# Optimization experiments

Hardware: AMD Instinct MI355X
Metric: run time of the kernel (lower is better)

The kernel has to match this reference:

```python
import jax, jax.numpy as jnp
import numpy as np

B, N, T, F = 8, 2000, 64, 32
H = 128    # lstm_hidden
GH = 128   # gnn_hidden
E = 32000  # edges


def setup_inputs() -> dict:
    key = jax.random.key(0)
    ks = jax.random.split(key, 12)
    s = 0.05
    return {
        "x": jax.random.normal(ks[0], (B, N, T, F), jnp.float32),
        "edge_index": jax.random.randint(ks[1], (2, E), 0, N, dtype=jnp.int32),
        # LSTM params (torch gate order i, f, g, o)
        "Wih": jax.random.normal(ks[2], (4 * H, F), jnp.float32) * s,
        "Whh": jax.random.normal(ks[3], (4 * H, H), jnp.float32) * s,
        "bih": jax.random.normal(ks[4], (4 * H,), jnp.float32) * s,
        "bhh": jax.random.normal(ks[5], (4 * H,), jnp.float32) * s,
        # GCNConv params
        "gcn_W": jax.random.normal(ks[6], (H, GH), jnp.float32) * s,
        "gcn_b": jax.random.normal(ks[7], (GH,), jnp.float32) * s,
        # shared MLP head
        "mlp_W1": jax.random.normal(ks[8], (GH, GH // 2), jnp.float32) * s,
        "mlp_b1": jax.random.normal(ks[9], (GH // 2,), jnp.float32) * s,
        "mlp_W2": jax.random.normal(ks[10], (GH // 2, 1), jnp.float32) * s,
        "mlp_b2": jax.random.normal(ks[11], (1,), jnp.float32) * s,
    }


def _lstm_last_h(x, Wih, Whh, bih, bhh):
    # x: [M, T, F] -> last hidden state [M, H]
    M = x.shape[0]
    xg = jnp.einsum('mtf,gf->mtg', x, Wih) + bih  # precompute input gates [M, T, 4H]

    def step(carry, xg_t):
        h, c = carry
        z = xg_t + h @ Whh.T + bhh
        i, f, g, o = jnp.split(z, 4, axis=-1)
        i = jax.nn.sigmoid(i)
        f = jax.nn.sigmoid(f)
        g = jnp.tanh(g)
        o = jax.nn.sigmoid(o)
        c = f * c + i * g
        h = o * jnp.tanh(c)
        return (h, c), None

    h0 = jnp.zeros((M, H), x.dtype)
    c0 = jnp.zeros((M, H), x.dtype)
    (h, _), _ = jax.lax.scan(step, (h0, c0), jnp.swapaxes(xg, 0, 1))
    return h


def reference(x, edge_index, Wih, Whh, bih, bhh, gcn_W, gcn_b,
              mlp_W1, mlp_b1, mlp_W2, mlp_b2):
    Bx, Nx, Tx, Fx = x.shape
    # LSTM over all B*N node sequences, take last hidden state
    h = _lstm_last_h(x.reshape(Bx * Nx, Tx, Fx), Wih, Whh, bih, bhh)
    node_features = h.reshape(Bx, Nx, H)

    # GCNConv (PyG semantics): add self-loops, symmetric normalization
    loops = jnp.arange(Nx, dtype=edge_index.dtype)
    src = jnp.concatenate([edge_index[0], loops])
    dst = jnp.concatenate([edge_index[1], loops])
    deg = jnp.zeros((Nx,), x.dtype).at[dst].add(1.0)
    dinv = jnp.where(deg > 0, jax.lax.rsqrt(deg), 0.0)
    norm = dinv[src] * dinv[dst]  # [E+N]

    xw = node_features @ gcn_W                     # [B, N, GH]
    msgs = xw[:, src, :] * norm[None, :, None]     # gather + scale [B, E+N, GH]
    agg = jnp.zeros((Bx, Nx, GH), x.dtype).at[:, dst, :].add(msgs) + gcn_b

    # shared MLP head (dropout is identity in eval mode)
    h1 = jax.nn.silu(agg @ mlp_W1 + mlp_b1)
    out = h1 @ mlp_W2 + mlp_b2                     # [B, N, 1]
    return out.squeeze(-1)                         # [B, N]
```

## Files before the change

kernel.cpp:

```cpp
#include <hip/hip_runtime.h>

typedef _Float16 f16x8 __attribute__((ext_vector_type(8)));
typedef _Float16 f16x4 __attribute__((ext_vector_type(4)));
typedef _Float16 f16x2 __attribute__((ext_vector_type(2)));
typedef float f32x4 __attribute__((ext_vector_type(4)));

#define NB_   8
#define NN_   2000
#define TT_   64
#define FF_   32
#define HH_   128
#define EE_   32000
#define KD    160
#define RSTR  192
#define NODES 32
#define WXSTR 40

__device__ __forceinline__ float fexp2(float v) { return __builtin_amdgcn_exp2f(v); }
__device__ __forceinline__ float frcp(float v)  { return __builtin_amdgcn_rcpf(v); }

__global__ void prep_kernel(const float* __restrict__ Wih, const float* __restrict__ Whh,
                            const float* __restrict__ bih, const float* __restrict__ bhh,
                            const float* __restrict__ gcnW,
                            _Float16* __restrict__ W16, _Float16* __restrict__ Wg16,
                            float* __restrict__ bias, float* __restrict__ deg) {
  int idx = blockIdx.x * 256 + threadIdx.x;
  if (idx < 512 * KD) {
    int col = idx / KD, k = idx % KD;
    float v = (k < 32) ? Wih[col * 32 + k] : Whh[col * 128 + (k - 32)];
    float sc = (col >= 256 && col < 384) ? -2.88539008f : -1.44269504f;
    W16[idx] = (_Float16)(v * sc);
  } else if (idx < 512 * KD + 128 * 128) {
    int i2 = idx - 512 * KD;
    int colg = i2 >> 7, k = i2 & 127;
    Wg16[i2] = (_Float16)gcnW[k * 128 + colg];
  } else if (idx < 512 * KD + 128 * 128 + 512) {
    int i3 = idx - (512 * KD + 128 * 128);
    float sc = (i3 >= 256 && i3 < 384) ? -2.88539008f : -1.44269504f;
    bias[i3] = (bih[i3] + bhh[i3]) * sc;
  } else if (idx < 512 * KD + 128 * 128 + 512 + NN_) {
    deg[idx - (512 * KD + 128 * 128 + 512)] = 0.f;
  }
}

__global__ void deg_kernel(const int* __restrict__ ei, float* __restrict__ deg) {
  int e = blockIdx.x * 256 + threadIdx.x;
  if (e < EE_ + NN_) {
    int d = (e < EE_) ? ei[EE_ + e] : (e - EE_);
    atomicAdd(&deg[d], 1.f);
  }
}

__global__ void scan_kernel(const float* __restrict__ deg, int* __restrict__ offs,
                            int* __restrict__ cursor, float* __restrict__ dinv) {
  __shared__ int s0[2048], s1[2048];
  int t = threadIdx.x;
  for (int i = t; i < 2048; i += 1024) s0[i] = (i < NN_) ? ((int)deg[i] - 1) : 0;
  __syncthreads();
  int* src = s0; int* dst = s1;
  for (int off = 1; off < 2048; off <<= 1) {
    for (int i = t; i < 2048; i += 1024)
      dst[i] = src[i] + ((i >= off) ? src[i - off] : 0);
    __syncthreads();
    int* tmp = src; src = dst; dst = tmp;
  }
  for (int i = t; i < NN_; i += 1024) {
    int exc = src[i] - ((int)deg[i] - 1);
    offs[i] = exc;
    cursor[i] = exc;
    float d = deg[i];
    dinv[i] = (d > 0.f) ? __builtin_amdgcn_rsqf(d) : 0.f;
  }
}

__global__ void fill_kernel(const int* __restrict__ ei, const float* __restrict__ dinv,
                            int* __restrict__ cursor, int* __restrict__ csr_src,
                            float* __restrict__ csr_w) {
  int e = blockIdx.x * 256 + threadIdx.x;
  if (e >= EE_) return;
  int s = ei[e], d = ei[EE_ + e];
  int pos = atomicAdd(&cursor[d], 1);
  csr_src[pos] = s;
  csr_w[pos] = dinv[s] * dinv[d];
}

__global__ __launch_bounds__(512, 4) void lstm_gcn_kernel(
    const float* __restrict__ x, const _Float16* __restrict__ W16,
    const float* __restrict__ bias, const _Float16* __restrict__ Wg16,
    float* __restrict__ xwT) {
  __shared__ _Float16 A[NODES * RSTR];
  __shared__ _Float16 WxL[512 * WXSTR];
  __shared__ float    BiasL[512];
  const int tid  = threadIdx.x;
  const int wave = tid >> 6;
  const int lane = tid & 63;
  const int n15  = lane & 15;
  const int q    = lane >> 4;
  const int m    = n15 & 7;
  const int hm   = m >> 2;
  const int qx   = q ^ (m & 3);
  const int node0 = blockIdx.x * NODES;

  f16x8 Af[4][4];
#pragma unroll
  for (int g = 0; g < 4; ++g) {
    const int row = g * 128 + wave * 16 + n15;
#pragma unroll
    for (int kc = 1; kc < 5; ++kc)
      Af[g][kc - 1] = *(const f16x8*)(W16 + row * KD + kc * 32 + q * 8);
  }
  {
    const _Float16* wr = W16 + tid * KD;
#pragma unroll
    for (int cch = 0; cch < 4; ++cch)
      *(f16x8*)(WxL + tid * WXSTR + cch * 8) = *(const f16x8*)(wr + cch * 8);
    if (tid < 128) *(float4*)(BiasL + tid * 4) = *(const float4*)(bias + tid * 4);
  }

  const int bRow = n15 * RSTR + (qx << 3);
  const int hOff = n15 * RSTR + (((4 + 2 * wave + (q >> 1)) ^ m) << 3) + ((q & 1) << 2);
  const int aRow = (wave * 16 + n15) * WXSTR + q * 8;

  const int xrow = tid >> 4;
  const int xf   = (tid & 15) * 2;
  const int xOff = xrow * RSTR + (((xf >> 3) ^ (xrow & 7)) << 3) + (xf & 7);
  const float* xb = x + (size_t)(node0 + xrow) * (TT_ * FF_) + xf;

  {
    int row = tid >> 4, ci = tid & 15;
    f16x8 z8 = {(_Float16)0, (_Float16)0, (_Float16)0, (_Float16)0,
                (_Float16)0, (_Float16)0, (_Float16)0, (_Float16)0};
    *(f16x8*)(A + row * RSTR + (((4 + ci) ^ (row & 7)) << 3)) = z8;
  }
  {
    float2 v = *(const float2*)xb;
    f16x2 p = {(_Float16)v.x, (_Float16)v.y};
    *(f16x2*)(A + xOff) = p;
  }
  __syncthreads();

  f32x4 acc[2][4], c[2];
  c[0] = (f32x4){0, 0, 0, 0};
  c[1] = (f32x4){0, 0, 0, 0};

  for (int t = 0; t < TT_; ++t) {
    {
      f32x4 bt[4];
#pragma unroll
      for (int g = 0; g < 4; ++g)
        bt[g] = *(const f32x4*)(BiasL + g * 128 + wave * 16 + q * 4);
#pragma unroll
      for (int nt = 0; nt < 2; ++nt)
#pragma unroll
        for (int g = 0; g < 4; ++g) acc[nt][g] = bt[g];
      f16x8 ax[4];
#pragma unroll
      for (int g = 0; g < 4; ++g)
        ax[g] = *(const f16x8*)(WxL + g * 128 * WXSTR + aRow);
#pragma unroll
      for (int nt = 0; nt < 2; ++nt) {
        f16x8 bf = *(const f16x8*)(A + nt * (16 * RSTR) + bRow + (hm << 5));
#pragma unroll
        for (int g = 0; g < 4; ++g)
          acc[nt][g] = __builtin_amdgcn_mfma_f32_16x16x32_f16(ax[g], bf, acc[nt][g], 0, 0, 0);
      }
#pragma unroll
      for (int kc = 1; kc < 5; ++kc)
#pragma unroll
        for (int nt = 0; nt < 2; ++nt) {
          f16x8 bf = *(const f16x8*)(A + nt * (16 * RSTR) + bRow + ((kc ^ hm) << 5));
#pragma unroll
          for (int g = 0; g < 4; ++g)
            acc[nt][g] = __builtin_amdgcn_mfma_f32_16x16x32_f16(Af[g][kc - 1], bf, acc[nt][g], 0, 0, 0);
        }
    }
    const bool more = (t + 1 < TT_);
    float2 xv;
    if (more) xv = *(const float2*)(xb + (t + 1) * FF_);
    __syncthreads();

#pragma unroll
    for (int nt = 0; nt < 2; ++nt) {
      f16x4 hp;
#pragma unroll
      for (int r = 0; r < 4; ++r) {
        float si = frcp(1.f + fexp2(acc[nt][0][r]));
        float sf = frcp(1.f + fexp2(acc[nt][1][r]));
        float tg = 2.f * frcp(1.f + fexp2(acc[nt][2][r])) - 1.f;
        float so = frcp(1.f + fexp2(acc[nt][3][r]));
        float cn = sf * c[nt][r] + si * tg;
        c[nt][r] = cn;
        float tc = 2.f * frcp(1.f + fexp2(-2.88539008f * cn)) - 1.f;
        hp[r] = (_Float16)(so * tc);
      }
      *(f16x4*)(A + nt * (16 * RSTR) + hOff) = hp;
    }
    if (more) { f16x2 p = {(_Float16)xv.x, (_Float16)xv.y}; *(f16x2*)(A + xOff) = p; }
    __syncthreads();
  }

  f16x8 Ag[4];
#pragma unroll
  for (int kc = 0; kc < 4; ++kc)
    Ag[kc] = *(const f16x8*)(Wg16 + (wave * 16 + n15) * HH_ + kc * 32 + q * 8);
  f32x4 acc2[2];
  acc2[0] = (f32x4){0, 0, 0, 0};
  acc2[1] = (f32x4){0, 0, 0, 0};
#pragma unroll
  for (int kc = 0; kc < 4; ++kc)
#pragma unroll
    for (int nt = 0; nt < 2; ++nt) {
      f16x8 bf = *(const f16x8*)(A + nt * (16 * RSTR) + bRow + (((kc + 1) ^ hm) << 5));
      acc2[nt] = __builtin_amdgcn_mfma_f32_16x16x32_f16(Ag[kc], bf, acc2[nt], 0, 0, 0);
    }
#pragma unroll
  for (int nt = 0; nt < 2; ++nt) {
    int mnode = node0 + nt * 16 + n15;
    int b = mnode / NN_;
    int n = mnode - b * NN_;
    *(float4*)(xwT + ((size_t)n * 8 + b) * HH_ + wave * 16 + q * 4) =
        (float4){acc2[nt][0], acc2[nt][1], acc2[nt][2], acc2[nt][3]};
  }
}

__global__ __launch_bounds__(256) void gathermlp_kernel(
    const float* __restrict__ xwT, const int* __restrict__ offs,
    const float* __restrict__ deg, const float* __restrict__ dinv,
    const int* __restrict__ csr_src, const float* __restrict__ csr_w,
    const float* __restrict__ gcnb,
    const float* __restrict__ W1, const float* __restrict__ b1,
    const float* __restrict__ W2, const float* __restrict__ b2,
    float* __restrict__ out) {
  __shared__ float aggs[8][128];
  __shared__ float W1T[64][132];
  const int d = blockIdx.x;
  const int tid = threadIdx.x;
  for (int i = tid; i < 8192; i += 256) {
    int k = i >> 6, j = i & 63;
    W1T[j][k] = W1[i];
  }
  {
    const int j  = tid & 127;
    const int bh = tid >> 7;
    const int beg = offs[d];
    const int cnt = (int)deg[d] - 1;
    const int boff = bh * 512 + j;
    float a0 = 0.f, a1 = 0.f, a2 = 0.f, a3 = 0.f;
    int e = 0;
    for (; e + 1 < cnt; e += 2) {
      int s0 = csr_src[beg + e],     s1 = csr_src[beg + e + 1];
      float w0 = csr_w[beg + e],     w1 = csr_w[beg + e + 1];
      const float* p0 = xwT + (size_t)s0 * 1024 + boff;
      const float* p1 = xwT + (size_t)s1 * 1024 + boff;
      float v00 = p0[0], v01 = p0[128], v02 = p0[256], v03 = p0[384];
      float v10 = p1[0], v11 = p1[128], v12 = p1[256], v13 = p1[384];
      a0 += w0 * v00 + w1 * v10;
      a1 += w0 * v01 + w1 * v11;
      a2 += w0 * v02 + w1 * v12;
      a3 += w0 * v03 + w1 * v13;
    }
    if (e < cnt) {
      int s = csr_src[beg + e];
      float w = csr_w[beg + e];
      const float* p = xwT + (size_t)s * 1024 + boff;
      a0 += w * p[0]; a1 += w * p[128]; a2 += w * p[256]; a3 += w * p[384];
    }
    {
      float di = dinv[d];
      float w = di * di;
      const float* p = xwT + (size_t)d * 1024 + boff;
      a0 += w * p[0]; a1 += w * p[128]; a2 += w * p[256]; a3 += w * p[384];
    }
    float bj = gcnb[j];
    aggs[bh * 4 + 0][j] = a0 + bj;
    aggs[bh * 4 + 1][j] = a1 + bj;
    aggs[bh * 4 + 2][j] = a2 + bj;
    aggs[bh * 4 + 3][j] = a3 + bj;
  }
  __syncthreads();
  const int b = tid >> 5;
  const int t = tid & 31;
  float acc1 = b1[t], acc2 = b1[t + 32];
#pragma unroll 8
  for (int kc = 0; kc < 32; ++kc) {
    float4 a  = *(const float4*)&aggs[b][kc * 4];
    float4 w1 = *(const float4*)&W1T[t][kc * 4];
    float4 w2 = *(const float4*)&W1T[t + 32][kc * 4];
    acc1 += a.x * w1.x + a.y * w1.y + a.z * w1.z + a.w * w1.w;
    acc2 += a.x * w2.x + a.y * w2.y + a.z * w2.z + a.w * w2.w;
  }
  float s1 = acc1 * frcp(1.f + fexp2(-1.44269504f * acc1));
  float s2 = acc2 * frcp(1.f + fexp2(-1.44269504f * acc2));
  float part = s1 * W2[t] + s2 * W2[t + 32];
#pragma unroll
  for (int msk = 16; msk >= 1; msk >>= 1) part += __shfl_xor(part, msk);
  if (t == 0) out[(size_t)b * NN_ + d] = part + b2[0];
}

extern "C" void kernel_launch(void* const* d_in, const int* in_sizes, int n_in,
                              void* d_out, int out_size, void* d_ws, size_t ws_size,
                              hipStream_t stream) {
  const float* x    = (const float*)d_in[0];
  const int*   ei   = (const int*)d_in[1];
  const float* Wih  = (const float*)d_in[2];
  const float* Whh  = (const float*)d_in[3];
  const float* bih  = (const float*)d_in[4];
  const float* bhh  = (const float*)d_in[5];
  const float* gcnW = (const float*)d_in[6];
  const float* gcnb = (const float*)d_in[7];
  const float* W1   = (const float*)d_in[8];
  const float* b1   = (const float*)d_in[9];
  const float* W2   = (const float*)d_in[10];
  const float* b2   = (const float*)d_in[11];
  float* out = (float*)d_out;
  char* ws = (char*)d_ws;

  _Float16* W16    = (_Float16*)(ws);
  _Float16* Wg16   = (_Float16*)(ws + 163840);
  float*    bias   = (float*)(ws + 196608);
  float*    xwT    = (float*)(ws + 198656);
  float*    deg    = (float*)(ws + 8390656);
  float*    dinv   = (float*)(ws + 8398848);
  int*      offs   = (int*)(ws + 8407040);
  int*      cursor = (int*)(ws + 8415232);
  int*      csrs   = (int*)(ws + 8423424);
  float*    csrw   = (float*)(ws + 8551424);

  prep_kernel<<<394, 256, 0, stream>>>(Wih, Whh, bih, bhh, gcnW, W16, Wg16, bias, deg);
  deg_kernel<<<133, 256, 0, stream>>>(ei, deg);
  scan_kernel<<<1, 1024, 0, stream>>>(deg, offs, cursor, dinv);
  fill_kernel<<<125, 256, 0, stream>>>(ei, dinv, cursor, csrs, csrw);
  lstm_gcn_kernel<<<500, 512, 0, stream>>>(x, W16, bias, Wg16, xwT);
  gathermlp_kernel<<<NN_, 256, 0, stream>>>(xwT, offs, deg, dinv, csrs, csrw,
                                            gcnb, W1, b1, W2, b2, out);
}
```

Measured before the change: 407.9 us.

## Double-buffer LSTM state in LDS, keep weights in registers, vectorize GCN gather

The LSTM kernel now ping-pongs the recurrent activation tile between two LDS buffers, so each timestep needs one barrier instead of two. The input-projection weight slice and the bias move from LDS into registers, which removes per-step LDS reads but raises register pressure. The xwT layout changes to node-major with batch innermost, so the gather kernel loads four batch values per edge with one 16-byte load. It also unrolls the edge loop by four for more memory parallelism, while the LSTM epilogue now writes scalar strided stores.

```diff
diff --git a/kernel.cpp b/kernel.cpp
--- a/kernel.cpp
+++ b/kernel.cpp
@@ -14,7 +14,7 @@
 #define KD    160
 #define RSTR  192
 #define NODES 32
-#define WXSTR 40
+#define BUFE  (NODES * RSTR)
 
 __device__ __forceinline__ float fexp2(float v) { return __builtin_amdgcn_exp2f(v); }
 __device__ __forceinline__ float frcp(float v)  { return __builtin_amdgcn_rcpf(v); }
@@ -88,9 +88,7 @@
     const float* __restrict__ x, const _Float16* __restrict__ W16,
     const float* __restrict__ bias, const _Float16* __restrict__ Wg16,
     float* __restrict__ xwT) {
-  __shared__ _Float16 A[NODES * RSTR];
-  __shared__ _Float16 WxL[512 * WXSTR];
-  __shared__ float    BiasL[512];
+  __shared__ _Float16 A[2 * BUFE];
   const int tid  = threadIdx.x;
   const int wave = tid >> 6;
   const int lane = tid & 63;
@@ -101,25 +99,19 @@
   const int qx   = q ^ (m & 3);
   const int node0 = blockIdx.x * NODES;
 
-  f16x8 Af[4][4];
+  f16x8 Af[4][5];
+  f32x4 bt[4];
 #pragma unroll
   for (int g = 0; g < 4; ++g) {
     const int row = g * 128 + wave * 16 + n15;
 #pragma unroll
-    for (int kc = 1; kc < 5; ++kc)
-      Af[g][kc - 1] = *(const f16x8*)(W16 + row * KD + kc * 32 + q * 8);
-  }
-  {
-    const _Float16* wr = W16 + tid * KD;
-#pragma unroll
-    for (int cch = 0; cch < 4; ++cch)
-      *(f16x8*)(WxL + tid * WXSTR + cch * 8) = *(const f16x8*)(wr + cch * 8);
-    if (tid < 128) *(float4*)(BiasL + tid * 4) = *(const float4*)(bias + tid * 4);
+    for (int kc = 0; kc < 5; ++kc)
+      Af[g][kc] = *(const f16x8*)(W16 + row * KD + kc * 32 + q * 8);
+    bt[g] = *(const f32x4*)(bias + g * 128 + wave * 16 + q * 4);
   }
 
   const int bRow = n15 * RSTR + (qx << 3);
   const int hOff = n15 * RSTR + (((4 + 2 * wave + (q >> 1)) ^ m) << 3) + ((q & 1) << 2);
-  const int aRow = (wave * 16 + n15) * WXSTR + q * 8;
 
   const int xrow = tid >> 4;
   const int xf   = (tid & 15) * 2;
@@ -131,53 +123,44 @@
     f16x8 z8 = {(_Float16)0, (_Float16)0, (_Float16)0, (_Float16)0,
                 (_Float16)0, (_Float16)0, (_Float16)0, (_Float16)0};
     *(f16x8*)(A + row * RSTR + (((4 + ci) ^ (row & 7)) << 3)) = z8;
-  }
-  {
     float2 v = *(const float2*)xb;
     f16x2 p = {(_Float16)v.x, (_Float16)v.y};
     *(f16x2*)(A + xOff) = p;
   }
   __syncthreads();
 
-  f32x4 acc[2][4], c[2];
+  f32x4 c[2];
   c[0] = (f32x4){0, 0, 0, 0};
   c[1] = (f32x4){0, 0, 0, 0};
 
   for (int t = 0; t < TT_; ++t) {
-    {
-      f32x4 bt[4];
-#pragma unroll
-      for (int g = 0; g < 4; ++g)
-        bt[g] = *(const f32x4*)(BiasL + g * 128 + wave * 16 + q * 4);
-#pragma unroll
-      for (int nt = 0; nt < 2; ++nt)
-#pragma unroll
-        for (int g = 0; g < 4; ++g) acc[nt][g] = bt[g];
-      f16x8 ax[4];
-#pragma unroll
-      for (int g = 0; g < 4; ++g)
-        ax[g] = *(const f16x8*)(WxL + g * 128 * WXSTR + aRow);
-#pragma unroll
-      for (int nt = 0; nt < 2; ++nt) {
-        f16x8 bf = *(const f16x8*)(A + nt * (16 * RSTR) + bRow + (hm << 5));
-#pragma unroll
-        for (int g = 0; g < 4; ++g)
-          acc[nt][g] = __builtin_amdgcn_mfma_f32_16x16x32_f16(ax[g], bf, acc[nt][g], 0, 0, 0);
-      }
-#pragma unroll
-      for (int kc = 1; kc < 5; ++kc)
-#pragma unroll
-        for (int nt = 0; nt < 2; ++nt) {
-          f16x8 bf = *(const f16x8*)(A + nt * (16 * RSTR) + bRow + ((kc ^ hm) << 5));
-#pragma unroll
-          for (int g = 0; g < 4; ++g)
-            acc[nt][g] = __builtin_amdgcn_mfma_f32_16x16x32_f16(Af[g][kc - 1], bf, acc[nt][g], 0, 0, 0);
-        }
-    }
+    const _Float16* src = A + (t & 1) * BUFE;
+    _Float16*       dst = A + ((t + 1) & 1) * BUFE;
     const bool more = (t + 1 < TT_);
     float2 xv;
     if (more) xv = *(const float2*)(xb + (t + 1) * FF_);
-    __syncthreads();
+
+    f32x4 acc[2][4];
+    {
+      f16x8 bf0[2];
+#pragma unroll
+      for (int nt = 0; nt < 2; ++nt)
+        bf0[nt] = *(const f16x8*)(src + nt * (16 * RSTR) + bRow + (hm << 5));
+#pragma unroll
+      for (int nt = 0; nt < 2; ++nt)
+#pragma unroll
+        for (int g = 0; g < 4; ++g)
+          acc[nt][g] = __builtin_amdgcn_mfma_f32_16x16x32_f16(Af[g][0], bf0[nt], bt[g], 0, 0, 0);
+#pragma unroll
+      for (int kc = 1; kc < 5; ++kc)
+#pragma unroll
+        for (int nt = 0; nt < 2; ++nt) {
+          f16x8 bf = *(const f16x8*)(src + nt * (16 * RSTR) + bRow + ((kc ^ hm) << 5));
+#pragma unroll
+          for (int g = 0; g < 4; ++g)
+            acc[nt][g] = __builtin_amdgcn_mfma_f32_16x16x32_f16(Af[g][kc], bf, acc[nt][g], 0, 0, 0);
+        }
+    }
 
 #pragma unroll
     for (int nt = 0; nt < 2; ++nt) {
@@ -193,9 +176,9 @@
         float tc = 2.f * frcp(1.f + fexp2(-2.88539008f * cn)) - 1.f;
         hp[r] = (_Float16)(so * tc);
       }
-      *(f16x4*)(A + nt * (16 * RSTR) + hOff) = hp;
-    }
-    if (more) { f16x2 p = {(_Float16)xv.x, (_Float16)xv.y}; *(f16x2*)(A + xOff) = p; }
+      *(f16x4*)(dst + nt * (16 * RSTR) + hOff) = hp;
+    }
+    if (more) { f16x2 p = {(_Float16)xv.x, (_Float16)xv.y}; *(f16x2*)(dst + xOff) = p; }
     __syncthreads();
   }
 
@@ -218,8 +201,11 @@
     int mnode = node0 + nt * 16 + n15;
     int b = mnode / NN_;
     int n = mnode - b * NN_;
-    *(float4*)(xwT + ((size_t)n * 8 + b) * HH_ + wave * 16 + q * 4) =
-        (float4){acc2[nt][0], acc2[nt][1], acc2[nt][2], acc2[nt][3]};
+    float* o = xwT + (size_t)n * 1024 + (wave * 16 + q * 4) * 8 + b;
+    o[0]  = acc2[nt][0];
+    o[8]  = acc2[nt][1];
+    o[16] = acc2[nt][2];
+    o[24] = acc2[nt][3];
   }
 }
 
@@ -235,47 +221,40 @@
   __shared__ float W1T[64][132];
   const int d = blockIdx.x;
   const int tid = threadIdx.x;
-  for (int i = tid; i < 8192; i += 256) {
-    int k = i >> 6, j = i & 63;
-    W1T[j][k] = W1[i];
-  }
+  for (int i = tid; i < 8192; i += 256) W1T[i & 63][i >> 6] = W1[i];
   {
     const int j  = tid & 127;
     const int bh = tid >> 7;
     const int beg = offs[d];
     const int cnt = (int)deg[d] - 1;
-    const int boff = bh * 512 + j;
-    float a0 = 0.f, a1 = 0.f, a2 = 0.f, a3 = 0.f;
+    const float* base = xwT + j * 8 + bh * 4;
+    f32x4 a = (f32x4){0, 0, 0, 0};
     int e = 0;
-    for (; e + 1 < cnt; e += 2) {
-      int s0 = csr_src[beg + e],     s1 = csr_src[beg + e + 1];
-      float w0 = csr_w[beg + e],     w1 = csr_w[beg + e + 1];
-      const float* p0 = xwT + (size_t)s0 * 1024 + boff;
-      const float* p1 = xwT + (size_t)s1 * 1024 + boff;
-      float v00 = p0[0], v01 = p0[128], v02 = p0[256], v03 = p0[384];
-      float v10 = p1[0], v11 = p1[128], v12 = p1[256], v13 = p1[384];
-      a0 += w0 * v00 + w1 * v10;
-      a1 += w0 * v01 + w1 * v11;
-      a2 += w0 * v02 + w1 * v12;
-      a3 += w0 * v03 + w1 * v13;
-    }
-    if (e < cnt) {
+    for (; e + 3 < cnt; e += 4) {
+      int   s0 = csr_src[beg + e],     s1 = csr_src[beg + e + 1];
+      int   s2 = csr_src[beg + e + 2], s3 = csr_src[beg + e + 3];
+      float w0 = csr_w[beg + e],       w1 = csr_w[beg + e + 1];
+      float w2 = csr_w[beg + e + 2],   w3 = csr_w[beg + e + 3];
+      f32x4 v0 = *(const f32x4*)(base + (size_t)s0 * 1024);
+      f32x4 v1 = *(const f32x4*)(base + (size_t)s1 * 1024);
+      f32x4 v2 = *(const f32x4*)(base + (size_t)s2 * 1024);
+      f32x4 v3 = *(const f32x4*)(base + (size_t)s3 * 1024);
+      a += w0 * v0 + w1 * v1 + w2 * v2 + w3 * v3;
+    }
+    for (; e < cnt; ++e) {
       int s = csr_src[beg + e];
       float w = csr_w[beg + e];
-      const float* p = xwT + (size_t)s * 1024 + boff;
-      a0 += w * p[0]; a1 += w * p[128]; a2 += w * p[256]; a3 += w * p[384];
+      a += w * *(const f32x4*)(base + (size_t)s * 1024);
     }
     {
       float di = dinv[d];
-      float w = di * di;
-      const float* p = xwT + (size_t)d * 1024 + boff;
-      a0 += w * p[0]; a1 += w * p[128]; a2 += w * p[256]; a3 += w * p[384];
+      a += (di * di) * *(const f32x4*)(base + (size_t)d * 1024);
     }
     float bj = gcnb[j];
-    aggs[bh * 4 + 0][j] = a0 + bj;
-    aggs[bh * 4 + 1][j] = a1 + bj;
-    aggs[bh * 4 + 2][j] = a2 + bj;
-    aggs[bh * 4 + 3][j] = a3 + bj;
+    aggs[bh * 4 + 0][j] = a[0] + bj;
+    aggs[bh * 4 + 1][j] = a[1] + bj;
+    aggs[bh * 4 + 2][j] = a[2] + bj;
+    aggs[bh * 4 + 3][j] = a[3] + bj;
   }
   __syncthreads();
   const int b = tid >> 5;
```

Result: slower. 664.6 us (+62.9%).
